# Optimization experiments

Measured on AMD Instinct MI355X. Metric: run time of the kernel, lower is better.

## Reference

```python
import jax, jax.numpy as jnp
import numpy as np

H = 128          # h_dim
N_NODES = 100000
N_EDGES = 1600000
N_GRAPHS = 256
EPS_BN = 1e-5


def setup_inputs() -> dict:
    key = jax.random.key(0)
    ks = jax.random.split(key, 12)
    x = jax.random.normal(ks[0], (N_NODES, 4), dtype=jnp.float32)
    edge_index = jax.random.randint(ks[1], (2, N_EDGES), 0, N_NODES, dtype=jnp.int64)
    batch = jnp.sort(jax.random.randint(ks[2], (N_NODES,), 0, N_GRAPHS, dtype=jnp.int64))
    # Linear weights (xavier-ish scale), stored as [in, out]
    W1 = jax.random.normal(ks[3], (4, H), dtype=jnp.float32) * (1.0 / np.sqrt(4))
    W2 = jax.random.normal(ks[4], (H, H), dtype=jnp.float32) * (1.0 / np.sqrt(H))
    W3 = jax.random.normal(ks[5], (H, H), dtype=jnp.float32) * (1.0 / np.sqrt(H))
    Wfc = jax.random.normal(ks[6], (H, 1), dtype=jnp.float32) * (1.0 / np.sqrt(H))
    def bn_params(k):
        k1, k2, k3, k4 = jax.random.split(k, 4)
        gamma = 1.0 + 0.1 * jax.random.normal(k1, (H,), dtype=jnp.float32)
        beta = 0.1 * jax.random.normal(k2, (H,), dtype=jnp.float32)
        mean = 0.1 * jax.random.normal(k3, (H,), dtype=jnp.float32)
        var = 1.0 + 0.1 * jax.random.uniform(k4, (H,), dtype=jnp.float32)
        return gamma, beta, mean, var
    g1, b1, m1, v1 = bn_params(ks[7])
    g2, b2, m2, v2 = bn_params(ks[8])
    g3, b3, m3, v3 = bn_params(ks[9])
    return {
        "x": x, "edge_index": edge_index, "batch": batch,
        "W1": W1, "g1": g1, "b1": b1, "m1": m1, "v1": v1,
        "W2": W2, "g2": g2, "b2": b2, "m2": m2, "v2": v2,
        "W3": W3, "g3": g3, "b3": b3, "m3": m3, "v3": v3,
        "Wfc": Wfc,
    }


def _gin_layer(h, src, dst, W, gamma, beta, mean, var):
    # GINConv with eps=0: mlp(x + sum_{j in N(i)} x_j)
    aggr = jax.ops.segment_sum(h[src], dst, num_segments=N_NODES)
    z = (h + aggr) @ W                                  # Linear(bias=False)
    z = (z - mean) * (gamma / jnp.sqrt(var + EPS_BN)) + beta  # BatchNorm1d (eval)
    return jax.nn.relu(z)


def reference(x, edge_index, batch,
              W1, g1, b1, m1, v1,
              W2, g2, b2, m2, v2,
              W3, g3, b3, m3, v3,
              Wfc):
    src, dst = edge_index[0], edge_index[1]
    h = _gin_layer(x, src, dst, W1, g1, b1, m1, v1)
    h = _gin_layer(h, src, dst, W2, g2, b2, m2, v2)
    h = _gin_layer(h, src, dst, W3, g3, b3, m3, v3)
    # dropout: identity in eval mode
    sums = jax.ops.segment_sum(h, batch, num_segments=N_GRAPHS)      # [G, H]
    cnts = jax.ops.segment_sum(jnp.ones((N_NODES, 1), h.dtype), batch,
                               num_segments=N_GRAPHS)                # [G, 1]
    pooled = sums / jnp.maximum(cnts, 1.0)
    return jax.nn.sigmoid(pooled @ Wfc)                               # [G, 1]
```

## Files before the change

### kernel.cpp

```cpp
#include <hip/hip_runtime.h>
#include <hip/hip_fp8.h>
#include <math.h>

#define N_NODES 100000
#define N_EDGES 1600000
#define N_GRAPHS 256
#define H 128
#define EPS_BN 1e-5f
#define ELLW 64

#define PSZ 256
#define PSH 8
#define P_PART 391
#define BLD_NBLK 200
#define EPT 32
#define EPB_A (256 * EPT)

typedef unsigned int uint;
typedef unsigned short ushort;
typedef __attribute__((ext_vector_type(8))) short bf16x8;
typedef __attribute__((ext_vector_type(4))) float f32x4;
typedef __attribute__((ext_vector_type(2))) float f32x2;
typedef __attribute__((ext_vector_type(4))) int i32x4;
typedef __attribute__((ext_vector_type(2))) int i32x2;

__device__ __forceinline__ uint f2bf_bits(float x) {
    uint u = __float_as_uint(x);
    return (u + 0x7fffu + ((u >> 16) & 1u)) >> 16;
}
__device__ __forceinline__ uint pack_bf2(float a, float b) {
    return f2bf_bits(a) | (f2bf_bits(b) << 16);
}
__device__ __forceinline__ float bf_lo(uint p) { return __uint_as_float(p << 16); }
__device__ __forceinline__ float bf_hi(uint p) { return __uint_as_float(p & 0xffff0000u); }

__device__ __forceinline__ unsigned char f32_to_fp8(float x) {
#if __has_builtin(__builtin_amdgcn_cvt_pk_fp8_f32)
    int v = __builtin_amdgcn_cvt_pk_fp8_f32(x, 0.0f, 0, false);
    return (unsigned char)(v & 0xff);
#else
    __hip_fp8_e4m3 q(x);
    return (unsigned char)q.__x;
#endif
}
__device__ __forceinline__ f32x4 fp8x4_to_f32x4(uint v) {
    f32x4 r;
#if __has_builtin(__builtin_amdgcn_cvt_pk_f32_fp8)
    f32x2 lo = __builtin_amdgcn_cvt_pk_f32_fp8((int)v, false);
    f32x2 hi = __builtin_amdgcn_cvt_pk_f32_fp8((int)v, true);
    r.x = lo.x; r.y = lo.y; r.z = hi.x; r.w = hi.y;
#else
    __hip_fp8_e4m3 a, b, c, d;
    a.__x = (unsigned char)(v & 0xff);
    b.__x = (unsigned char)((v >> 8) & 0xff);
    c.__x = (unsigned char)((v >> 16) & 0xff);
    d.__x = (unsigned char)((v >> 24) & 0xff);
    r.x = (float)a; r.y = (float)b; r.z = (float)c; r.w = (float)d;
#endif
    return r;
}

__global__ __launch_bounds__(256) void k_hist(const int* __restrict__ dst,
                                              int* __restrict__ hist,
                                              const int* __restrict__ batch,
                                              int* __restrict__ gstart,
                                              const float* __restrict__ W2,
                                              ushort* __restrict__ Wpk2,
                                              const float* __restrict__ W3,
                                              ushort* __restrict__ Wpk3,
                                              float* __restrict__ Gz) {
    __shared__ int h[P_PART];
    int b = blockIdx.x;
    if (b < BLD_NBLK) {
        for (int i = threadIdx.x; i < P_PART; i += 256) h[i] = 0;
        __syncthreads();
        int base = b * EPB_A + threadIdx.x * EPT;
        #pragma unroll
        for (int j = 0; j < EPT / 4; j++) {
            int e = base + j * 4;
            if (e + 4 <= N_EDGES) {
                i32x4 d = __builtin_nontemporal_load((const i32x4*)&dst[e]);
                atomicAdd(&h[d.x >> PSH], 1);
                atomicAdd(&h[d.y >> PSH], 1);
                atomicAdd(&h[d.z >> PSH], 1);
                atomicAdd(&h[d.w >> PSH], 1);
            }
        }
        __syncthreads();
        for (int i = threadIdx.x; i < P_PART; i += 256)
            hist[b * P_PART + i] = h[i];
        return;
    }
    if (b < 592) {
        int n = (b - 200) * 256 + threadIdx.x;
        if (n >= N_NODES) return;
        int g = batch[n];
        int gp = (n == 0) ? -1 : batch[n - 1];
        for (int gr = gp + 1; gr <= g; gr++) gstart[gr] = n;
        if (n == N_NODES - 1) {
            for (int gr = g + 1; gr <= N_GRAPHS; gr++) gstart[gr] = N_NODES;
        }
        return;
    }
    if (b >= 608) {
        if (threadIdx.x < N_GRAPHS) Gz[threadIdx.x] = 0.0f;
        return;
    }
    const float* W = (b < 600) ? W2 : W3;
    ushort* Wpk = (b < 600) ? Wpk2 : Wpk3;
    int t = ((b < 600) ? (b - 592) : (b - 600)) * 256 + threadIdx.x;
    int lane = t & 63, nt = (t >> 6) & 7, kt = t >> 9;
    int n = nt * 16 + (lane & 15);
    int kbase = kt * 32 + (lane >> 4) * 8;
    ushort v[8];
    #pragma unroll
    for (int j = 0; j < 8; j++)
        v[j] = (ushort)f2bf_bits(W[(size_t)(kbase + j) * H + n]);
    uint4 pk;
    pk.x = (uint)v[0] | ((uint)v[1] << 16);
    pk.y = (uint)v[2] | ((uint)v[3] << 16);
    pk.z = (uint)v[4] | ((uint)v[5] << 16);
    pk.w = (uint)v[6] | ((uint)v[7] << 16);
    *(uint4*)&Wpk[(size_t)t * 8] = pk;
}

__global__ __launch_bounds__(256) void k_scan_a(const int* __restrict__ hist,
                                                int* __restrict__ offs,
                                                int* __restrict__ tot) {
    __shared__ int lds[256];
    int p = blockIdx.x;
    int t = threadIdx.x;
    int v = (t < BLD_NBLK) ? hist[t * P_PART + p] : 0;
    lds[t] = v;
    __syncthreads();
    for (int off = 1; off < 256; off <<= 1) {
        int tmp = (t >= off) ? lds[t - off] : 0;
        __syncthreads();
        lds[t] += tmp;
        __syncthreads();
    }
    if (t < BLD_NBLK) offs[t * P_PART + p] = lds[t] - v;
    if (t == 255) tot[p] = lds[255];
}

__global__ void k_scan_b(const int* __restrict__ tot, int* __restrict__ parr) {
    __shared__ int lds[512];
    int p = threadIdx.x;
    int v = (p < P_PART) ? tot[p] : 0;
    lds[p] = v;
    __syncthreads();
    for (int off = 1; off < 512; off <<= 1) {
        int tmp = (p >= off) ? lds[p - off] : 0;
        __syncthreads();
        lds[p] += tmp;
        __syncthreads();
    }
    if (p < P_PART) parr[p] = lds[p] - v;
    if (p == 0) parr[P_PART] = N_EDGES;
}

__global__ __launch_bounds__(256) void k_scatter(const int* __restrict__ src,
                                                 const int* __restrict__ dst,
                                                 const int* __restrict__ offs,
                                                 const int* __restrict__ parr,
                                                 i32x2* __restrict__ ebuf) {
    __shared__ int lofs[P_PART];
    for (int i = threadIdx.x; i < P_PART; i += 256)
        lofs[i] = offs[blockIdx.x * P_PART + i] + parr[i];
    __syncthreads();
    int base = blockIdx.x * EPB_A + threadIdx.x * EPT;
    #pragma unroll
    for (int j = 0; j < EPT / 4; j++) {
        int e = base + j * 4;
        if (e + 4 <= N_EDGES) {
            i32x4 d = __builtin_nontemporal_load((const i32x4*)&dst[e]);
            i32x4 s = __builtin_nontemporal_load((const i32x4*)&src[e]);
            #pragma unroll
            for (int k = 0; k < 4; k++) {
                int dk = (k == 0) ? d.x : (k == 1) ? d.y : (k == 2) ? d.z : d.w;
                int sk = (k == 0) ? s.x : (k == 1) ? s.y : (k == 2) ? s.z : s.w;
                int pos = atomicAdd(&lofs[dk >> PSH], 1);
                i32x2 sd; sd.x = sk; sd.y = dk;
                ebuf[pos] = sd;
            }
        }
    }
}

__global__ __launch_bounds__(256) void k_build(const i32x2* __restrict__ ebuf,
                                               const int* __restrict__ parr,
                                               int* __restrict__ cnt,
                                               int* __restrict__ ell) {
    __shared__ int lc[PSZ];
    int p = blockIdx.x;
    for (int i = threadIdx.x; i < PSZ; i += 256) lc[i] = 0;
    __syncthreads();
    int e0 = parr[p], e1 = parr[p + 1];
    for (int i = e0 + threadIdx.x; i < e1; i += 256) {
        i32x2 sd = ebuf[i];
        int d = sd.y;
        int slot = atomicAdd(&lc[d & (PSZ - 1)], 1);
        if (slot < ELLW) ell[(size_t)d * ELLW + slot] = sd.x;
    }
    __syncthreads();
    int nb = p * PSZ;
    for (int i = threadIdx.x; i < PSZ; i += 256) {
        int n = nb + i;
        if (n < N_NODES) cnt[n] = lc[i];
    }
}

__global__ __launch_bounds__(256) void k_layer1(
    const float* __restrict__ x, const int* __restrict__ cnt,
    const int* __restrict__ ell, const float* __restrict__ W1,
    const float* __restrict__ gamma, const float* __restrict__ beta,
    const float* __restrict__ mean, const float* __restrict__ var,
    uint* __restrict__ Hf8) {
    __shared__ float scs[128], shs[128];
    int tid = threadIdx.x;
    if (tid < 128) {
        float sc = gamma[tid] * rsqrtf(var[tid] + EPS_BN);
        scs[tid] = sc;
        shs[tid] = beta[tid] - mean[tid] * sc;
    }
    __syncthreads();
    int lane = tid & 63, wave = tid >> 6;
    int sub = lane >> 4, m = lane & 15;
    int n = blockIdx.x * 16 + wave * 4 + sub;
    if (n >= N_NODES) return;
    int cn = cnt[n]; if (cn > ELLW) cn = ELLW;
    const int* row = &ell[(size_t)n * ELLW];
    float4 acc = {0.f, 0.f, 0.f, 0.f};
    for (int e = m; e < cn; e += 16) {
        float4 v = *(const float4*)&x[(size_t)row[e] * 4];
        acc.x += v.x; acc.y += v.y; acc.z += v.z; acc.w += v.w;
    }
    #pragma unroll
    for (int off = 8; off > 0; off >>= 1) {
        acc.x += __shfl_down(acc.x, off, 16);
        acc.y += __shfl_down(acc.y, off, 16);
        acc.z += __shfl_down(acc.z, off, 16);
        acc.w += __shfl_down(acc.w, off, 16);
    }
    int src = lane & 48;
    float4 xs = *(const float4*)&x[(size_t)n * 4];
    float uu[4];
    uu[0] = __shfl(acc.x, src, 64) + xs.x;
    uu[1] = __shfl(acc.y, src, 64) + xs.y;
    uu[2] = __shfl(acc.z, src, 64) + xs.z;
    uu[3] = __shfl(acc.w, src, 64) + xs.w;
    int j0 = m * 8;
    float z[8] = {0.f, 0.f, 0.f, 0.f, 0.f, 0.f, 0.f, 0.f};
    #pragma unroll
    for (int k = 0; k < 4; k++) {
        float4 wa = *(const float4*)&W1[k * H + j0];
        float4 wb = *(const float4*)&W1[k * H + j0 + 4];
        z[0] += uu[k] * wa.x; z[1] += uu[k] * wa.y;
        z[2] += uu[k] * wa.z; z[3] += uu[k] * wa.w;
        z[4] += uu[k] * wb.x; z[5] += uu[k] * wb.y;
        z[6] += uu[k] * wb.z; z[7] += uu[k] * wb.w;
    }
    #pragma unroll
    for (int i = 0; i < 8; i++)
        z[i] = fmaxf(z[i] * scs[j0 + i] + shs[j0 + i], 0.0f);
    uint2 q;
    q.x = (uint)f32_to_fp8(z[0]) | ((uint)f32_to_fp8(z[1]) << 8)
        | ((uint)f32_to_fp8(z[2]) << 16) | ((uint)f32_to_fp8(z[3]) << 24);
    q.y = (uint)f32_to_fp8(z[4]) | ((uint)f32_to_fp8(z[5]) << 8)
        | ((uint)f32_to_fp8(z[6]) << 16) | ((uint)f32_to_fp8(z[7]) << 24);
    *(uint2*)&Hf8[(size_t)n * 32 + m * 2] = q;
}

__global__ __launch_bounds__(256) void k_aggr128(
    const uint* __restrict__ Hf8, const int* __restrict__ cnt,
    const int* __restrict__ ell, uint* __restrict__ Ubf) {
    int t = blockIdx.x * 256 + threadIdx.x;
    int n = t >> 6, lane = t & 63;
    if (n >= N_NODES) return;
    int half = lane >> 5, c4 = lane & 31;
    float a0 = 0.f, a1 = 0.f, a2 = 0.f, a3 = 0.f;
    int cn = cnt[n]; if (cn > ELLW) cn = ELLW;
    const int* row = &ell[(size_t)n * ELLW];
    int e = half;
    for (; e + 14 < cn; e += 16) {
        int s0 = row[e + 0], s1 = row[e + 2], s2 = row[e + 4], s3 = row[e + 6];
        int s4 = row[e + 8], s5 = row[e + 10], s6 = row[e + 12], s7 = row[e + 14];
        uint p0 = Hf8[(size_t)s0 * 32 + c4];
        uint p1 = Hf8[(size_t)s1 * 32 + c4];
        uint p2 = Hf8[(size_t)s2 * 32 + c4];
        uint p3 = Hf8[(size_t)s3 * 32 + c4];
        uint p4 = Hf8[(size_t)s4 * 32 + c4];
        uint p5 = Hf8[(size_t)s5 * 32 + c4];
        uint p6 = Hf8[(size_t)s6 * 32 + c4];
        uint p7 = Hf8[(size_t)s7 * 32 + c4];
        f32x4 f0 = fp8x4_to_f32x4(p0), f1 = fp8x4_to_f32x4(p1);
        f32x4 f2 = fp8x4_to_f32x4(p2), f3 = fp8x4_to_f32x4(p3);
        f32x4 f4 = fp8x4_to_f32x4(p4), f5 = fp8x4_to_f32x4(p5);
        f32x4 f6 = fp8x4_to_f32x4(p6), f7 = fp8x4_to_f32x4(p7);
        a0 += (f0.x + f1.x + f2.x + f3.x) + (f4.x + f5.x + f6.x + f7.x);
        a1 += (f0.y + f1.y + f2.y + f3.y) + (f4.y + f5.y + f6.y + f7.y);
        a2 += (f0.z + f1.z + f2.z + f3.z) + (f4.z + f5.z + f6.z + f7.z);
        a3 += (f0.w + f1.w + f2.w + f3.w) + (f4.w + f5.w + f6.w + f7.w);
    }
    for (; e + 6 < cn; e += 8) {
        int s0 = row[e + 0], s1 = row[e + 2], s2 = row[e + 4], s3 = row[e + 6];
        uint p0 = Hf8[(size_t)s0 * 32 + c4];
        uint p1 = Hf8[(size_t)s1 * 32 + c4];
        uint p2 = Hf8[(size_t)s2 * 32 + c4];
        uint p3 = Hf8[(size_t)s3 * 32 + c4];
        f32x4 f0 = fp8x4_to_f32x4(p0), f1 = fp8x4_to_f32x4(p1);
        f32x4 f2 = fp8x4_to_f32x4(p2), f3 = fp8x4_to_f32x4(p3);
        a0 += f0.x + f1.x + f2.x + f3.x;
        a1 += f0.y + f1.y + f2.y + f3.y;
        a2 += f0.z + f1.z + f2.z + f3.z;
        a3 += f0.w + f1.w + f2.w + f3.w;
    }
    for (; e < cn; e += 2) {
        f32x4 f = fp8x4_to_f32x4(Hf8[(size_t)row[e] * 32 + c4]);
        a0 += f.x; a1 += f.y; a2 += f.z; a3 += f.w;
    }
    a0 += __shfl_down(a0, 32, 64);
    a1 += __shfl_down(a1, 32, 64);
    a2 += __shfl_down(a2, 32, 64);
    a3 += __shfl_down(a3, 32, 64);
    if (half == 0) {
        f32x4 sf = fp8x4_to_f32x4(Hf8[(size_t)n * 32 + c4]);
        a0 += sf.x; a1 += sf.y; a2 += sf.z; a3 += sf.w;
        uint2 ov; ov.x = pack_bf2(a0, a1); ov.y = pack_bf2(a2, a3);
        *(uint2*)&Ubf[(size_t)n * 64 + c4 * 2] = ov;
    }
}

__global__ __launch_bounds__(256) void k_gemm_mfma(
    const uint* __restrict__ Ubf, const uint* __restrict__ Wpk,
    const float* __restrict__ gamma, const float* __restrict__ beta,
    const float* __restrict__ mean, const float* __restrict__ var,
    unsigned char* __restrict__ Hf8,
    const int* __restrict__ batch, const float* __restrict__ Wfc,
    float* __restrict__ Gz, int mode) {
    __shared__ uint lds_u[64 * 68];
    __shared__ float wfc[128];
    __shared__ int bb[64];
    __shared__ float sblk[64];
    int tid = threadIdx.x;
    int row0 = blockIdx.x * 64;
    if (mode == 2) {
        if (tid < 128) wfc[tid] = Wfc[tid];
        if (tid < 64) {
            int rr = row0 + tid;
            bb[tid] = (rr < N_NODES) ? batch[rr] : -1;
        }
    }
    #pragma unroll
    for (int it = 0; it < 4; it++) {
        int r = it * 16 + (tid >> 4);
        int c = (tid & 15) * 4;
        int gr = row0 + r; if (gr >= N_NODES) gr = N_NODES - 1;
        uint4 v = *(const uint4*)&Ubf[(size_t)gr * 64 + c];
        *(uint4*)&lds_u[r * 68 + c] = v;
    }
    __syncthreads();

    int wave = tid >> 6, lane = tid & 63;
    int m = lane & 15, quad = lane >> 4;
    bf16x8 a[4];
    #pragma unroll
    for (int kt = 0; kt < 4; kt++)
        a[kt] = *(const bf16x8*)&lds_u[(wave * 16 + m) * 68 + kt * 16 + quad * 4];

    f32x4 acc[8];
    #pragma unroll
    for (int nt = 0; nt < 8; nt++) acc[nt] = (f32x4){0.f, 0.f, 0.f, 0.f};

    #pragma unroll
    for (int nt = 0; nt < 8; nt++) {
        #pragma unroll
        for (int kt = 0; kt < 4; kt++) {
            bf16x8 b = *(const bf16x8*)&Wpk[((size_t)(kt * 8 + nt) * 64 + lane) * 4];
            acc[nt] = __builtin_amdgcn_mfma_f32_16x16x32_bf16(a[kt], b, acc[nt], 0, 0, 0);
        }
    }

    if (mode == 1) {
        #pragma unroll
        for (int nt = 0; nt < 8; nt++) {
            int col = nt * 16 + m;
            float sc = gamma[col] * rsqrtf(var[col] + EPS_BN);
            float sh = beta[col] - mean[col] * sc;
            #pragma unroll
            for (int r = 0; r < 4; r++) {
                int row = row0 + wave * 16 + quad * 4 + r;
                if (row < N_NODES) {
                    float z = fmaxf(acc[nt][r] * sc + sh, 0.0f);
                    Hf8[(size_t)row * 128 + col] = f32_to_fp8(z);
                }
            }
        }
    } else {
        float pr[4] = {0.f, 0.f, 0.f, 0.f};
        #pragma unroll
        for (int nt = 0; nt < 8; nt++) {
            int col = nt * 16 + m;
            float sc = gamma[col] * rsqrtf(var[col] + EPS_BN);
            float sh = beta[col] - mean[col] * sc;
            float wf = wfc[col];
            #pragma unroll
            for (int r = 0; r < 4; r++) {
                float z = fmaxf(acc[nt][r] * sc + sh, 0.0f);
                pr[r] += z * wf;
            }
        }
        #pragma unroll
        for (int r = 0; r < 4; r++) {
            float p = pr[r];
            p += __shfl_down(p, 8, 16);
            p += __shfl_down(p, 4, 16);
            p += __shfl_down(p, 2, 16);
            p += __shfl_down(p, 1, 16);
            if (m == 0) sblk[wave * 16 + quad * 4 + r] = p;
        }
        __syncthreads();
        if (tid == 0) {
            int i = 0;
            while (i < 64 && row0 + i < N_NODES) {
                int g = bb[i];
                float s = 0.0f;
                while (i < 64 && row0 + i < N_NODES && bb[i] == g) {
                    s += sblk[i]; i++;
                }
                atomicAdd(&Gz[g], s);
            }
        }
    }
}

__global__ void k_fc(const float* __restrict__ Gz, const int* __restrict__ gstart,
                     float* __restrict__ out) {
    int g = threadIdx.x;
    if (g < N_GRAPHS) {
        int c = gstart[g + 1] - gstart[g];
        float z = Gz[g] / fmaxf((float)c, 1.0f);
        out[g] = 1.0f / (1.0f + expf(-z));
    }
}

extern "C" void kernel_launch(void* const* d_in, const int* in_sizes, int n_in,
                              void* d_out, int out_size, void* d_ws, size_t ws_size,
                              hipStream_t stream) {
    const float* x     = (const float*)d_in[0];
    const int*   ei    = (const int*)d_in[1];
    const int*   batch = (const int*)d_in[2];
    const float* W1    = (const float*)d_in[3];
    const float* g1    = (const float*)d_in[4];
    const float* b1    = (const float*)d_in[5];
    const float* m1    = (const float*)d_in[6];
    const float* v1    = (const float*)d_in[7];
    const float* W2    = (const float*)d_in[8];
    const float* g2    = (const float*)d_in[9];
    const float* b2    = (const float*)d_in[10];
    const float* m2    = (const float*)d_in[11];
    const float* v2    = (const float*)d_in[12];
    const float* W3    = (const float*)d_in[13];
    const float* g3    = (const float*)d_in[14];
    const float* b3    = (const float*)d_in[15];
    const float* m3    = (const float*)d_in[16];
    const float* v3    = (const float*)d_in[17];
    const float* Wfc   = (const float*)d_in[18];
    float* out = (float*)d_out;

    const int* srcp = ei;
    const int* dstp = ei + N_EDGES;

    uint* Ubf  = (uint*)d_ws;
    uint* Hf8u = Ubf + (size_t)N_NODES * 64;
    int* cnt   = (int*)(Hf8u + (size_t)N_NODES * 32);
    int* ell   = cnt + N_NODES;
    int* gstart = ell + (size_t)N_NODES * ELLW;
    ushort* Wpk2 = (ushort*)(gstart + 260);
    ushort* Wpk3 = Wpk2 + 16384;
    int* hist  = (int*)(Wpk3 + 16384);
    int* offs  = hist + BLD_NBLK * P_PART;
    int* parr  = offs + BLD_NBLK * P_PART;
    int* tot   = parr + 400;
    float* Gz  = (float*)(tot + 400);
    i32x2* ebuf = (i32x2*)Ubf;

    k_hist<<<609, 256, 0, stream>>>(dstp, hist, batch, gstart, W2, Wpk2, W3, Wpk3, Gz);
    k_scan_a<<<P_PART, 256, 0, stream>>>(hist, offs, tot);
    k_scan_b<<<1, 512, 0, stream>>>(tot, parr);
    k_scatter<<<BLD_NBLK, 256, 0, stream>>>(srcp, dstp, offs, parr, ebuf);
    k_build<<<P_PART, 256, 0, stream>>>(ebuf, parr, cnt, ell);

    k_layer1<<<(N_NODES + 15) / 16, 256, 0, stream>>>(
        x, cnt, ell, W1, g1, b1, m1, v1, Hf8u);
    k_aggr128<<<(N_NODES * 64 + 255) / 256, 256, 0, stream>>>(Hf8u, cnt, ell, Ubf);
    k_gemm_mfma<<<(N_NODES + 63) / 64, 256, 0, stream>>>(
        Ubf, (const uint*)Wpk2, g2, b2, m2, v2, (unsigned char*)Hf8u,
        batch, Wfc, Gz, 1);
    k_aggr128<<<(N_NODES * 64 + 255) / 256, 256, 0, stream>>>(Hf8u, cnt, ell, Ubf);
    k_gemm_mfma<<<(N_NODES + 63) / 64, 256, 0, stream>>>(
        Ubf, (const uint*)Wpk3, g3, b3, m3, v3, (unsigned char*)Hf8u,
        batch, Wfc, Gz, 2);
    k_fc<<<1, 256, 0, stream>>>(Gz, gstart, out);
}
```

Before: 306.9 us.

## Fuse neighbor aggregation into MFMA GEMM kernel for layers 2 and 3

Merges the separate aggregation kernel and the MFMA GEMM kernel into one kernel per layer. Each wave gathers and sums neighbor fp8 features for its 16 rows and writes the bf16 sums straight into LDS, where the MFMA stage reads them. This removes the global bf16 intermediate buffer round trip and two kernel launches, and ping-pongs between two fp8 buffers. In exchange there is less parallelism per block during the gather (each wave walks its 16 nodes one after another), so latency hiding may suffer.

```diff
diff --git a/kernel.cpp b/kernel.cpp
--- a/kernel.cpp
+++ b/kernel.cpp
@@ -31,8 +31,6 @@
 __device__ __forceinline__ uint pack_bf2(float a, float b) {
     return f2bf_bits(a) | (f2bf_bits(b) << 16);
 }
-__device__ __forceinline__ float bf_lo(uint p) { return __uint_as_float(p << 16); }
-__device__ __forceinline__ float bf_hi(uint p) { return __uint_as_float(p & 0xffff0000u); }
 
 __device__ __forceinline__ unsigned char f32_to_fp8(float x) {
 #if __has_builtin(__builtin_amdgcn_cvt_pk_fp8_f32)
@@ -271,71 +269,12 @@
     *(uint2*)&Hf8[(size_t)n * 32 + m * 2] = q;
 }
 
-__global__ __launch_bounds__(256) void k_aggr128(
-    const uint* __restrict__ Hf8, const int* __restrict__ cnt,
-    const int* __restrict__ ell, uint* __restrict__ Ubf) {
-    int t = blockIdx.x * 256 + threadIdx.x;
-    int n = t >> 6, lane = t & 63;
-    if (n >= N_NODES) return;
-    int half = lane >> 5, c4 = lane & 31;
-    float a0 = 0.f, a1 = 0.f, a2 = 0.f, a3 = 0.f;
-    int cn = cnt[n]; if (cn > ELLW) cn = ELLW;
-    const int* row = &ell[(size_t)n * ELLW];
-    int e = half;
-    for (; e + 14 < cn; e += 16) {
-        int s0 = row[e + 0], s1 = row[e + 2], s2 = row[e + 4], s3 = row[e + 6];
-        int s4 = row[e + 8], s5 = row[e + 10], s6 = row[e + 12], s7 = row[e + 14];
-        uint p0 = Hf8[(size_t)s0 * 32 + c4];
-        uint p1 = Hf8[(size_t)s1 * 32 + c4];
-        uint p2 = Hf8[(size_t)s2 * 32 + c4];
-        uint p3 = Hf8[(size_t)s3 * 32 + c4];
-        uint p4 = Hf8[(size_t)s4 * 32 + c4];
-        uint p5 = Hf8[(size_t)s5 * 32 + c4];
-        uint p6 = Hf8[(size_t)s6 * 32 + c4];
-        uint p7 = Hf8[(size_t)s7 * 32 + c4];
-        f32x4 f0 = fp8x4_to_f32x4(p0), f1 = fp8x4_to_f32x4(p1);
-        f32x4 f2 = fp8x4_to_f32x4(p2), f3 = fp8x4_to_f32x4(p3);
-        f32x4 f4 = fp8x4_to_f32x4(p4), f5 = fp8x4_to_f32x4(p5);
-        f32x4 f6 = fp8x4_to_f32x4(p6), f7 = fp8x4_to_f32x4(p7);
-        a0 += (f0.x + f1.x + f2.x + f3.x) + (f4.x + f5.x + f6.x + f7.x);
-        a1 += (f0.y + f1.y + f2.y + f3.y) + (f4.y + f5.y + f6.y + f7.y);
-        a2 += (f0.z + f1.z + f2.z + f3.z) + (f4.z + f5.z + f6.z + f7.z);
-        a3 += (f0.w + f1.w + f2.w + f3.w) + (f4.w + f5.w + f6.w + f7.w);
-    }
-    for (; e + 6 < cn; e += 8) {
-        int s0 = row[e + 0], s1 = row[e + 2], s2 = row[e + 4], s3 = row[e + 6];
-        uint p0 = Hf8[(size_t)s0 * 32 + c4];
-        uint p1 = Hf8[(size_t)s1 * 32 + c4];
-        uint p2 = Hf8[(size_t)s2 * 32 + c4];
-        uint p3 = Hf8[(size_t)s3 * 32 + c4];
-        f32x4 f0 = fp8x4_to_f32x4(p0), f1 = fp8x4_to_f32x4(p1);
-        f32x4 f2 = fp8x4_to_f32x4(p2), f3 = fp8x4_to_f32x4(p3);
-        a0 += f0.x + f1.x + f2.x + f3.x;
-        a1 += f0.y + f1.y + f2.y + f3.y;
-        a2 += f0.z + f1.z + f2.z + f3.z;
-        a3 += f0.w + f1.w + f2.w + f3.w;
-    }
-    for (; e < cn; e += 2) {
-        f32x4 f = fp8x4_to_f32x4(Hf8[(size_t)row[e] * 32 + c4]);
-        a0 += f.x; a1 += f.y; a2 += f.z; a3 += f.w;
-    }
-    a0 += __shfl_down(a0, 32, 64);
-    a1 += __shfl_down(a1, 32, 64);
-    a2 += __shfl_down(a2, 32, 64);
-    a3 += __shfl_down(a3, 32, 64);
-    if (half == 0) {
-        f32x4 sf = fp8x4_to_f32x4(Hf8[(size_t)n * 32 + c4]);
-        a0 += sf.x; a1 += sf.y; a2 += sf.z; a3 += sf.w;
-        uint2 ov; ov.x = pack_bf2(a0, a1); ov.y = pack_bf2(a2, a3);
-        *(uint2*)&Ubf[(size_t)n * 64 + c4 * 2] = ov;
-    }
-}
-
-__global__ __launch_bounds__(256) void k_gemm_mfma(
-    const uint* __restrict__ Ubf, const uint* __restrict__ Wpk,
+__global__ __launch_bounds__(256) void k_layer23(
+    const uint* __restrict__ Hf8in, const int* __restrict__ cnt,
+    const int* __restrict__ ell, const uint* __restrict__ Wpk,
     const float* __restrict__ gamma, const float* __restrict__ beta,
     const float* __restrict__ mean, const float* __restrict__ var,
-    unsigned char* __restrict__ Hf8,
+    unsigned char* __restrict__ Hf8out,
     const int* __restrict__ batch, const float* __restrict__ Wfc,
     float* __restrict__ Gz, int mode) {
     __shared__ uint lds_u[64 * 68];
@@ -351,17 +290,74 @@
             bb[tid] = (rr < N_NODES) ? batch[rr] : -1;
         }
     }
-    #pragma unroll
-    for (int it = 0; it < 4; it++) {
-        int r = it * 16 + (tid >> 4);
-        int c = (tid & 15) * 4;
-        int gr = row0 + r; if (gr >= N_NODES) gr = N_NODES - 1;
-        uint4 v = *(const uint4*)&Ubf[(size_t)gr * 64 + c];
-        *(uint4*)&lds_u[r * 68 + c] = v;
-    }
-    __syncthreads();
 
     int wave = tid >> 6, lane = tid & 63;
+    int half = lane >> 5, c4 = lane & 31;
+
+    for (int i = 0; i < 16; i++) {
+        int r = wave * 16 + i;
+        int n = row0 + r;
+        float a0 = 0.f, a1 = 0.f, a2 = 0.f, a3 = 0.f;
+        if (n < N_NODES) {
+            int cn = cnt[n]; if (cn > ELLW) cn = ELLW;
+            const int* row = &ell[(size_t)n * ELLW];
+            int e = half;
+            for (; e + 14 < cn; e += 16) {
+                int s0 = row[e + 0], s1 = row[e + 2], s2 = row[e + 4], s3 = row[e + 6];
+                int s4 = row[e + 8], s5 = row[e + 10], s6 = row[e + 12], s7 = row[e + 14];
+                uint p0 = Hf8in[(size_t)s0 * 32 + c4];
+                uint p1 = Hf8in[(size_t)s1 * 32 + c4];
+                uint p2 = Hf8in[(size_t)s2 * 32 + c4];
+                uint p3 = Hf8in[(size_t)s3 * 32 + c4];
+                uint p4 = Hf8in[(size_t)s4 * 32 + c4];
+                uint p5 = Hf8in[(size_t)s5 * 32 + c4];
+                uint p6 = Hf8in[(size_t)s6 * 32 + c4];
+                uint p7 = Hf8in[(size_t)s7 * 32 + c4];
+                f32x4 f0 = fp8x4_to_f32x4(p0), f1 = fp8x4_to_f32x4(p1);
+                f32x4 f2 = fp8x4_to_f32x4(p2), f3 = fp8x4_to_f32x4(p3);
+                f32x4 f4 = fp8x4_to_f32x4(p4), f5 = fp8x4_to_f32x4(p5);
+                f32x4 f6 = fp8x4_to_f32x4(p6), f7 = fp8x4_to_f32x4(p7);
+                a0 += (f0.x + f1.x + f2.x + f3.x) + (f4.x + f5.x + f6.x + f7.x);
+                a1 += (f0.y + f1.y + f2.y + f3.y) + (f4.y + f5.y + f6.y + f7.y);
+                a2 += (f0.z + f1.z + f2.z + f3.z) + (f4.z + f5.z + f6.z + f7.z);
+                a3 += (f0.w + f1.w + f2.w + f3.w) + (f4.w + f5.w + f6.w + f7.w);
+            }
+            for (; e + 6 < cn; e += 8) {
+                int s0 = row[e + 0], s1 = row[e + 2], s2 = row[e + 4], s3 = row[e + 6];
+                uint p0 = Hf8in[(size_t)s0 * 32 + c4];
+                uint p1 = Hf8in[(size_t)s1 * 32 + c4];
+                uint p2 = Hf8in[(size_t)s2 * 32 + c4];
+                uint p3 = Hf8in[(size_t)s3 * 32 + c4];
+                f32x4 f0 = fp8x4_to_f32x4(p0), f1 = fp8x4_to_f32x4(p1);
+                f32x4 f2 = fp8x4_to_f32x4(p2), f3 = fp8x4_to_f32x4(p3);
+                a0 += f0.x + f1.x + f2.x + f3.x;
+                a1 += f0.y + f1.y + f2.y + f3.y;
+                a2 += f0.z + f1.z + f2.z + f3.z;
+                a3 += f0.w + f1.w + f2.w + f3.w;
+            }
+            for (; e < cn; e += 2) {
+                f32x4 f = fp8x4_to_f32x4(Hf8in[(size_t)row[e] * 32 + c4]);
+                a0 += f.x; a1 += f.y; a2 += f.z; a3 += f.w;
+            }
+        }
+        a0 += __shfl_down(a0, 32, 64);
+        a1 += __shfl_down(a1, 32, 64);
+        a2 += __shfl_down(a2, 32, 64);
+        a3 += __shfl_down(a3, 32, 64);
+        if (half == 0) {
+            float s0 = 0.f, s1 = 0.f, s2 = 0.f, s3 = 0.f;
+            if (n < N_NODES) {
+                f32x4 sf = fp8x4_to_f32x4(Hf8in[(size_t)n * 32 + c4]);
+                s0 = sf.x; s1 = sf.y; s2 = sf.z; s3 = sf.w;
+            }
+            uint2 ov;
+            ov.x = pack_bf2(a0 + s0, a1 + s1);
+            ov.y = pack_bf2(a2 + s2, a3 + s3);
+            *(uint2*)&lds_u[r * 68 + c4 * 2] = ov;
+        }
+    }
+    __syncthreads();
+
     int m = lane & 15, quad = lane >> 4;
     bf16x8 a[4];
     #pragma unroll
@@ -392,7 +388,7 @@
                 int row = row0 + wave * 16 + quad * 4 + r;
                 if (row < N_NODES) {
                     float z = fmaxf(acc[nt][r] * sc + sh, 0.0f);
-                    Hf8[(size_t)row * 128 + col] = f32_to_fp8(z);
+                    Hf8out[(size_t)row * 128 + col] = f32_to_fp8(z);
                 }
             }
         }
@@ -471,9 +467,9 @@
     const int* srcp = ei;
     const int* dstp = ei + N_EDGES;
 
-    uint* Ubf  = (uint*)d_ws;
-    uint* Hf8u = Ubf + (size_t)N_NODES * 64;
-    int* cnt   = (int*)(Hf8u + (size_t)N_NODES * 32);
+    uint* Hf8a = (uint*)d_ws;
+    uint* Hf8b = Hf8a + (size_t)N_NODES * 32;
+    int* cnt   = (int*)(Hf8b + (size_t)N_NODES * 32);
     int* ell   = cnt + N_NODES;
     int* gstart = ell + (size_t)N_NODES * ELLW;
     ushort* Wpk2 = (ushort*)(gstart + 260);
@@ -483,7 +479,7 @@
     int* parr  = offs + BLD_NBLK * P_PART;
     int* tot   = parr + 400;
     float* Gz  = (float*)(tot + 400);
-    i32x2* ebuf = (i32x2*)Ubf;
+    i32x2* ebuf = (i32x2*)(Gz + 256);
 
     k_hist<<<609, 256, 0, stream>>>(dstp, hist, batch, gstart, W2, Wpk2, W3, Wpk3, Gz);
     k_scan_a<<<P_PART, 256, 0, stream>>>(hist, offs, tot);
@@ -492,14 +488,12 @@
     k_build<<<P_PART, 256, 0, stream>>>(ebuf, parr, cnt, ell);
 
     k_layer1<<<(N_NODES + 15) / 16, 256, 0, stream>>>(
-        x, cnt, ell, W1, g1, b1, m1, v1, Hf8u);
-    k_aggr128<<<(N_NODES * 64 + 255) / 256, 256, 0, stream>>>(Hf8u, cnt, ell, Ubf);
-    k_gemm_mfma<<<(N_NODES + 63) / 64, 256, 0, stream>>>(
-        Ubf, (const uint*)Wpk2, g2, b2, m2, v2, (unsigned char*)Hf8u,
-        batch, Wfc, Gz, 1);
-    k_aggr128<<<(N_NODES * 64 + 255) / 256, 256, 0, stream>>>(Hf8u, cnt, ell, Ubf);
-    k_gemm_mfma<<<(N_NODES + 63) / 64, 256, 0, stream>>>(
-        Ubf, (const uint*)Wpk3, g3, b3, m3, v3, (unsigned char*)Hf8u,
-        batch, Wfc, Gz, 2);
+        x, cnt, ell, W1, g1, b1, m1, v1, Hf8a);
+    k_layer23<<<(N_NODES + 63) / 64, 256, 0, stream>>>(
+        Hf8a, cnt, ell, (const uint*)Wpk2, g2, b2, m2, v2,
+        (unsigned char*)Hf8b, batch, Wfc, Gz, 1);
+    k_layer23<<<(N_NODES + 63) / 64, 256, 0, stream>>>(
+        Hf8b, cnt, ell, (const uint*)Wpk3, g3, b3, m3, v3,
+        (unsigned char*)Hf8a, batch, Wfc, Gz, 2);
     k_fc<<<1, 256, 0, stream>>>(Gz, gstart, out);
 }
```

Result: slower. 374.8 us (+22.1%).

## Quantize node features to 4-bit with per-node scale for gather

Applied to the files above, without the earlier changes.

Replaces the FP8 node-feature storage with 4-bit unsigned nibbles plus a per-node float scale (max/15), produced in layer 1 and the mode-1 GEMM epilogue. The aggregation kernel now gathers 64 bytes per neighbor row instead of 128, which halves the random-access gather traffic. In exchange it adds an extra scale load per edge, more integer decode work per element, and a large precision loss that may break the accuracy tolerance.

```diff
diff --git a/kernel.cpp b/kernel.cpp
--- a/kernel.cpp
+++ b/kernel.cpp
@@ -1,5 +1,4 @@
 #include <hip/hip_runtime.h>
-#include <hip/hip_fp8.h>
 #include <math.h>
 
 #define N_NODES 100000
@@ -20,7 +19,6 @@
 typedef unsigned short ushort;
 typedef __attribute__((ext_vector_type(8))) short bf16x8;
 typedef __attribute__((ext_vector_type(4))) float f32x4;
-typedef __attribute__((ext_vector_type(2))) float f32x2;
 typedef __attribute__((ext_vector_type(4))) int i32x4;
 typedef __attribute__((ext_vector_type(2))) int i32x2;
 
@@ -31,33 +29,11 @@
 __device__ __forceinline__ uint pack_bf2(float a, float b) {
     return f2bf_bits(a) | (f2bf_bits(b) << 16);
 }
-__device__ __forceinline__ float bf_lo(uint p) { return __uint_as_float(p << 16); }
-__device__ __forceinline__ float bf_hi(uint p) { return __uint_as_float(p & 0xffff0000u); }
-
-__device__ __forceinline__ unsigned char f32_to_fp8(float x) {
-#if __has_builtin(__builtin_amdgcn_cvt_pk_fp8_f32)
-    int v = __builtin_amdgcn_cvt_pk_fp8_f32(x, 0.0f, 0, false);
-    return (unsigned char)(v & 0xff);
-#else
-    __hip_fp8_e4m3 q(x);
-    return (unsigned char)q.__x;
-#endif
-}
-__device__ __forceinline__ f32x4 fp8x4_to_f32x4(uint v) {
-    f32x4 r;
-#if __has_builtin(__builtin_amdgcn_cvt_pk_f32_fp8)
-    f32x2 lo = __builtin_amdgcn_cvt_pk_f32_fp8((int)v, false);
-    f32x2 hi = __builtin_amdgcn_cvt_pk_f32_fp8((int)v, true);
-    r.x = lo.x; r.y = lo.y; r.z = hi.x; r.w = hi.y;
-#else
-    __hip_fp8_e4m3 a, b, c, d;
-    a.__x = (unsigned char)(v & 0xff);
-    b.__x = (unsigned char)((v >> 8) & 0xff);
-    c.__x = (unsigned char)((v >> 16) & 0xff);
-    d.__x = (unsigned char)((v >> 24) & 0xff);
-    r.x = (float)a; r.y = (float)b; r.z = (float)c; r.w = (float)d;
-#endif
-    return r;
+
+__device__ __forceinline__ void dec4_acc(uint w, float q, float* a) {
+    #pragma unroll
+    for (int j = 0; j < 8; j++)
+        a[j] += (float)((w >> (4 * j)) & 15u) * q;
 }
 
 __global__ __launch_bounds__(256) void k_hist(const int* __restrict__ dst,
@@ -215,7 +191,7 @@
     const int* __restrict__ ell, const float* __restrict__ W1,
     const float* __restrict__ gamma, const float* __restrict__ beta,
     const float* __restrict__ mean, const float* __restrict__ var,
-    uint* __restrict__ Hf8) {
+    uint* __restrict__ H4, float* __restrict__ scl) {
     __shared__ float scs[128], shs[128];
     int tid = threadIdx.x;
     if (tid < 128) {
@@ -263,71 +239,66 @@
     #pragma unroll
     for (int i = 0; i < 8; i++)
         z[i] = fmaxf(z[i] * scs[j0 + i] + shs[j0 + i], 0.0f);
-    uint2 q;
-    q.x = (uint)f32_to_fp8(z[0]) | ((uint)f32_to_fp8(z[1]) << 8)
-        | ((uint)f32_to_fp8(z[2]) << 16) | ((uint)f32_to_fp8(z[3]) << 24);
-    q.y = (uint)f32_to_fp8(z[4]) | ((uint)f32_to_fp8(z[5]) << 8)
-        | ((uint)f32_to_fp8(z[6]) << 16) | ((uint)f32_to_fp8(z[7]) << 24);
-    *(uint2*)&Hf8[(size_t)n * 32 + m * 2] = q;
+    float lm = z[0];
+    #pragma unroll
+    for (int i = 1; i < 8; i++) lm = fmaxf(lm, z[i]);
+    #pragma unroll
+    for (int off = 1; off < 16; off <<= 1)
+        lm = fmaxf(lm, __shfl_xor(lm, off, 16));
+    float inv = (lm > 0.0f) ? 15.0f / lm : 0.0f;
+    if (m == 0) scl[n] = (lm > 0.0f) ? lm / 15.0f : 0.0f;
+    uint pk4 = 0;
+    #pragma unroll
+    for (int i = 0; i < 8; i++) {
+        uint nib = (uint)(z[i] * inv + 0.5f);
+        pk4 |= nib << (4 * i);
+    }
+    H4[(size_t)n * 16 + m] = pk4;
 }
 
 __global__ __launch_bounds__(256) void k_aggr128(
-    const uint* __restrict__ Hf8, const int* __restrict__ cnt,
-    const int* __restrict__ ell, uint* __restrict__ Ubf) {
+    const uint* __restrict__ H4, const float* __restrict__ scl,
+    const int* __restrict__ cnt, const int* __restrict__ ell,
+    uint* __restrict__ Ubf) {
     int t = blockIdx.x * 256 + threadIdx.x;
     int n = t >> 6, lane = t & 63;
     if (n >= N_NODES) return;
-    int half = lane >> 5, c4 = lane & 31;
-    float a0 = 0.f, a1 = 0.f, a2 = 0.f, a3 = 0.f;
+    int pair = lane >> 4, c = lane & 15;
+    float a[8] = {0.f, 0.f, 0.f, 0.f, 0.f, 0.f, 0.f, 0.f};
     int cn = cnt[n]; if (cn > ELLW) cn = ELLW;
     const int* row = &ell[(size_t)n * ELLW];
-    int e = half;
-    for (; e + 14 < cn; e += 16) {
-        int s0 = row[e + 0], s1 = row[e + 2], s2 = row[e + 4], s3 = row[e + 6];
-        int s4 = row[e + 8], s5 = row[e + 10], s6 = row[e + 12], s7 = row[e + 14];
-        uint p0 = Hf8[(size_t)s0 * 32 + c4];
-        uint p1 = Hf8[(size_t)s1 * 32 + c4];
-        uint p2 = Hf8[(size_t)s2 * 32 + c4];
-        uint p3 = Hf8[(size_t)s3 * 32 + c4];
-        uint p4 = Hf8[(size_t)s4 * 32 + c4];
-        uint p5 = Hf8[(size_t)s5 * 32 + c4];
-        uint p6 = Hf8[(size_t)s6 * 32 + c4];
-        uint p7 = Hf8[(size_t)s7 * 32 + c4];
-        f32x4 f0 = fp8x4_to_f32x4(p0), f1 = fp8x4_to_f32x4(p1);
-        f32x4 f2 = fp8x4_to_f32x4(p2), f3 = fp8x4_to_f32x4(p3);
-        f32x4 f4 = fp8x4_to_f32x4(p4), f5 = fp8x4_to_f32x4(p5);
-        f32x4 f6 = fp8x4_to_f32x4(p6), f7 = fp8x4_to_f32x4(p7);
-        a0 += (f0.x + f1.x + f2.x + f3.x) + (f4.x + f5.x + f6.x + f7.x);
-        a1 += (f0.y + f1.y + f2.y + f3.y) + (f4.y + f5.y + f6.y + f7.y);
-        a2 += (f0.z + f1.z + f2.z + f3.z) + (f4.z + f5.z + f6.z + f7.z);
-        a3 += (f0.w + f1.w + f2.w + f3.w) + (f4.w + f5.w + f6.w + f7.w);
-    }
-    for (; e + 6 < cn; e += 8) {
-        int s0 = row[e + 0], s1 = row[e + 2], s2 = row[e + 4], s3 = row[e + 6];
-        uint p0 = Hf8[(size_t)s0 * 32 + c4];
-        uint p1 = Hf8[(size_t)s1 * 32 + c4];
-        uint p2 = Hf8[(size_t)s2 * 32 + c4];
-        uint p3 = Hf8[(size_t)s3 * 32 + c4];
-        f32x4 f0 = fp8x4_to_f32x4(p0), f1 = fp8x4_to_f32x4(p1);
-        f32x4 f2 = fp8x4_to_f32x4(p2), f3 = fp8x4_to_f32x4(p3);
-        a0 += f0.x + f1.x + f2.x + f3.x;
-        a1 += f0.y + f1.y + f2.y + f3.y;
-        a2 += f0.z + f1.z + f2.z + f3.z;
-        a3 += f0.w + f1.w + f2.w + f3.w;
-    }
-    for (; e < cn; e += 2) {
-        f32x4 f = fp8x4_to_f32x4(Hf8[(size_t)row[e] * 32 + c4]);
-        a0 += f.x; a1 += f.y; a2 += f.z; a3 += f.w;
-    }
-    a0 += __shfl_down(a0, 32, 64);
-    a1 += __shfl_down(a1, 32, 64);
-    a2 += __shfl_down(a2, 32, 64);
-    a3 += __shfl_down(a3, 32, 64);
-    if (half == 0) {
-        f32x4 sf = fp8x4_to_f32x4(Hf8[(size_t)n * 32 + c4]);
-        a0 += sf.x; a1 += sf.y; a2 += sf.z; a3 += sf.w;
-        uint2 ov; ov.x = pack_bf2(a0, a1); ov.y = pack_bf2(a2, a3);
-        *(uint2*)&Ubf[(size_t)n * 64 + c4 * 2] = ov;
+    int e = pair;
+    for (; e + 12 < cn; e += 16) {
+        int s0 = row[e], s1 = row[e + 4], s2 = row[e + 8], s3 = row[e + 12];
+        uint w0 = H4[(size_t)s0 * 16 + c];
+        uint w1 = H4[(size_t)s1 * 16 + c];
+        uint w2 = H4[(size_t)s2 * 16 + c];
+        uint w3 = H4[(size_t)s3 * 16 + c];
+        float q0 = scl[s0], q1 = scl[s1], q2 = scl[s2], q3 = scl[s3];
+        dec4_acc(w0, q0, a);
+        dec4_acc(w1, q1, a);
+        dec4_acc(w2, q2, a);
+        dec4_acc(w3, q3, a);
+    }
+    for (; e < cn; e += 4) {
+        int s = row[e];
+        uint w = H4[(size_t)s * 16 + c];
+        float q = scl[s];
+        dec4_acc(w, q, a);
+    }
+    #pragma unroll
+    for (int j = 0; j < 8; j++) {
+        a[j] += __shfl_down(a[j], 32, 64);
+        a[j] += __shfl_down(a[j], 16, 64);
+    }
+    if (pair == 0) {
+        uint sw = H4[(size_t)n * 16 + c];
+        float sq = scl[n];
+        dec4_acc(sw, sq, a);
+        uint4 pk;
+        pk.x = pack_bf2(a[0], a[1]); pk.y = pack_bf2(a[2], a[3]);
+        pk.z = pack_bf2(a[4], a[5]); pk.w = pack_bf2(a[6], a[7]);
+        *(uint4*)&Ubf[(size_t)n * 64 + c * 4] = pk;
     }
 }
 
@@ -335,7 +306,7 @@
     const uint* __restrict__ Ubf, const uint* __restrict__ Wpk,
     const float* __restrict__ gamma, const float* __restrict__ beta,
     const float* __restrict__ mean, const float* __restrict__ var,
-    unsigned char* __restrict__ Hf8,
+    unsigned char* __restrict__ H4out, float* __restrict__ sclout,
     const int* __restrict__ batch, const float* __restrict__ Wfc,
     float* __restrict__ Gz, int mode) {
     __shared__ uint lds_u[64 * 68];
@@ -382,17 +353,36 @@
     }
 
     if (mode == 1) {
+        float zz[8][4];
         #pragma unroll
         for (int nt = 0; nt < 8; nt++) {
             int col = nt * 16 + m;
             float sc = gamma[col] * rsqrtf(var[col] + EPS_BN);
             float sh = beta[col] - mean[col] * sc;
             #pragma unroll
-            for (int r = 0; r < 4; r++) {
-                int row = row0 + wave * 16 + quad * 4 + r;
-                if (row < N_NODES) {
-                    float z = fmaxf(acc[nt][r] * sc + sh, 0.0f);
-                    Hf8[(size_t)row * 128 + col] = f32_to_fp8(z);
+            for (int r = 0; r < 4; r++)
+                zz[nt][r] = fmaxf(acc[nt][r] * sc + sh, 0.0f);
+        }
+        #pragma unroll
+        for (int r = 0; r < 4; r++) {
+            int rowr = row0 + wave * 16 + quad * 4 + r;
+            float lm = zz[0][r];
+            #pragma unroll
+            for (int nt = 1; nt < 8; nt++) lm = fmaxf(lm, zz[nt][r]);
+            #pragma unroll
+            for (int off = 1; off < 16; off <<= 1)
+                lm = fmaxf(lm, __shfl_xor(lm, off, 16));
+            float inv = (lm > 0.0f) ? 15.0f / lm : 0.0f;
+            if (rowr < N_NODES) {
+                if (m == 0) sclout[rowr] = (lm > 0.0f) ? lm / 15.0f : 0.0f;
+                #pragma unroll
+                for (int nt = 0; nt < 8; nt++) {
+                    uint nib = (uint)(zz[nt][r] * inv + 0.5f);
+                    uint nib2 = __shfl_down(nib, 1, 64);
+                    if ((m & 1) == 0) {
+                        H4out[(size_t)rowr * 64 + nt * 8 + (m >> 1)] =
+                            (unsigned char)(nib | (nib2 << 4));
+                    }
                 }
             }
         }
@@ -471,10 +461,13 @@
     const int* srcp = ei;
     const int* dstp = ei + N_EDGES;
 
-    uint* Ubf  = (uint*)d_ws;
-    uint* Hf8u = Ubf + (size_t)N_NODES * 64;
-    int* cnt   = (int*)(Hf8u + (size_t)N_NODES * 32);
-    int* ell   = cnt + N_NODES;
+    uint* Ubf   = (uint*)d_ws;
+    uint* H4a   = Ubf + (size_t)N_NODES * 64;
+    uint* H4b   = H4a + (size_t)N_NODES * 16;
+    float* scla = (float*)(H4b + (size_t)N_NODES * 16);
+    float* sclb = scla + N_NODES;
+    int* cnt    = (int*)(sclb + N_NODES);
+    int* ell    = cnt + N_NODES;
     int* gstart = ell + (size_t)N_NODES * ELLW;
     ushort* Wpk2 = (ushort*)(gstart + 260);
     ushort* Wpk3 = Wpk2 + 16384;
@@ -492,14 +485,14 @@
     k_build<<<P_PART, 256, 0, stream>>>(ebuf, parr, cnt, ell);
 
     k_layer1<<<(N_NODES + 15) / 16, 256, 0, stream>>>(
-        x, cnt, ell, W1, g1, b1, m1, v1, Hf8u);
-    k_aggr128<<<(N_NODES * 64 + 255) / 256, 256, 0, stream>>>(Hf8u, cnt, ell, Ubf);
+        x, cnt, ell, W1, g1, b1, m1, v1, H4a, scla);
+    k_aggr128<<<(N_NODES * 64 + 255) / 256, 256, 0, stream>>>(H4a, scla, cnt, ell, Ubf);
     k_gemm_mfma<<<(N_NODES + 63) / 64, 256, 0, stream>>>(
-        Ubf, (const uint*)Wpk2, g2, b2, m2, v2, (unsigned char*)Hf8u,
-        batch, Wfc, Gz, 1);
-    k_aggr128<<<(N_NODES * 64 + 255) / 256, 256, 0, stream>>>(Hf8u, cnt, ell, Ubf);
+        Ubf, (const uint*)Wpk2, g2, b2, m2, v2,
+        (unsigned char*)H4b, sclb, batch, Wfc, Gz, 1);
+    k_aggr128<<<(N_NODES * 64 + 255) / 256, 256, 0, stream>>>(H4b, sclb, cnt, ell, Ubf);
     k_gemm_mfma<<<(N_NODES + 63) / 64, 256, 0, stream>>>(
-        Ubf, (const uint*)Wpk3, g3, b3, m3, v3, (unsigned char*)Hf8u,
-        batch, Wfc, Gz, 2);
+        Ubf, (const uint*)Wpk3, g3, b3, m3, v3,
+        (unsigned char*)H4a, scla, batch, Wfc, Gz, 2);
     k_fc<<<1, 256, 0, stream>>>(Gz, gstart, out);
 }
```

Result: slower. 326.2 us (+6.3%).
